# Performance work log

Hardware: AMD Instinct MI355X
Metric: run time of the kernel (lower is better)

The kernel has to match this reference:

```python
import jax, jax.numpy as jnp
import numpy as np

D_INNER, D_STATE, DT_RANK, D_CONV, NBLK = 256, 8, 8, 4, 3

def _conv2d(x, w, b=None):
    y = jax.lax.conv_general_dilated(x, w, (1, 1), 'SAME', dimension_numbers=('NCHW', 'OIHW', 'NCHW'))
    return y if b is None else y + b[None, :, None, None]

def _ln(x, g, b, eps=1e-5):
    m = x.mean(-1, keepdims=True)
    v = x.var(-1, keepdims=True)
    return (x - m) / jnp.sqrt(v + eps) * g + b

def _bn(x, g, b, m, v, eps=1e-5):
    return (x - m[None, :, None, None]) / jnp.sqrt(v[None, :, None, None] + eps) * g[None, :, None, None] + b[None, :, None, None]

def _up2(x):
    return jnp.repeat(jnp.repeat(x, 2, axis=2), 2, axis=3)

def _silu(x):
    return x * jax.nn.sigmoid(x)

def _selective_scan(u, dt, A, Bm, Cm):
    # u, dt: (B,L,D); A: (D,N); Bm, Cm: (B,L,N)
    dA = jnp.exp(dt[..., None] * A)              # (B,L,D,N)
    dBu = (dt * u)[..., None] * Bm[:, :, None, :]
    h0 = jnp.zeros((u.shape[0], u.shape[2], A.shape[1]), u.dtype)
    def step(h, inp):
        dA_t, dBu_t, C_t = inp
        h = dA_t * h + dBu_t
        return h, jnp.einsum('bdn,bn->bd', h, C_t)
    _, ys = jax.lax.scan(step, h0, (jnp.moveaxis(dA, 1, 0), jnp.moveaxis(dBu, 1, 0), jnp.moveaxis(Cm, 1, 0)))
    return jnp.moveaxis(ys, 0, 1)                # (B,L,D)

def _mamba(x, in_w, conv_w, conv_b, xproj_w, dt_w, dt_b, Alog, Dp, out_w):
    xz = jnp.einsum('bld,ed->ble', x, in_w)      # (B,L,2*D_INNER)
    xm, z = jnp.split(xz, 2, axis=-1)
    xc = jnp.moveaxis(xm, 1, 2)                  # (B,D,L)
    xc = jax.lax.conv_general_dilated(xc, conv_w[:, None, :], (1,), [(D_CONV - 1, 0)], dimension_numbers=('NCH', 'OIH', 'NCH'), feature_group_count=D_INNER)
    xm = _silu(jnp.moveaxis(xc + conv_b[None, :, None], 2, 1))
    xdbl = jnp.einsum('bld,ed->ble', xm, xproj_w)
    dt, Bm, Cm = jnp.split(xdbl, [DT_RANK, DT_RANK + D_STATE], axis=-1)
    dt = jax.nn.softplus(jnp.einsum('blr,dr->bld', dt, dt_w) + dt_b)
    A = -jnp.exp(Alog)
    y = _selective_scan(xm, dt, A, Bm, Cm) + xm * Dp
    y = y * _silu(z)
    return jnp.einsum('bld,od->blo', y, out_w)

def _cce(inp, ref, w1, w2):
    a = _conv2d(inp, w1)
    r = _conv2d(ref, w2)
    gate = jax.nn.sigmoid(a.max(axis=(2, 3), keepdims=True) + a.mean(axis=(2, 3), keepdims=True))
    return r * gate


def setup_inputs() -> dict:
    key = jax.random.key(0)
    ks = jax.random.split(key, 24)
    s = 0.05
    inp = {}
    inp['fused'] = jax.random.normal(ks[0], (16, 1024, 128), jnp.float32)
    inp['orig_x'] = jax.random.uniform(ks[1], (16, 32, 128, 128), jnp.float32)
    inp['orig_y'] = jax.random.uniform(ks[2], (16, 32, 128, 128), jnp.float32)
    inp['m_ln_g'] = jnp.ones((NBLK, 128), jnp.float32)
    inp['m_ln_b'] = jnp.zeros((NBLK, 128), jnp.float32)
    inp['m_in_w'] = jax.random.normal(ks[3], (NBLK, 2 * D_INNER, 128), jnp.float32) * s
    inp['m_conv_w'] = jax.random.normal(ks[4], (NBLK, D_INNER, D_CONV), jnp.float32) * s
    inp['m_conv_b'] = jnp.zeros((NBLK, D_INNER), jnp.float32)
    inp['m_xproj_w'] = jax.random.normal(ks[5], (NBLK, DT_RANK + 2 * D_STATE, D_INNER), jnp.float32) * s
    inp['m_dt_w'] = jax.random.normal(ks[6], (NBLK, D_INNER, DT_RANK), jnp.float32) * s
    inp['m_dt_b'] = jax.random.normal(ks[7], (NBLK, D_INNER), jnp.float32) * 0.1
    inp['m_Alog'] = jnp.log(jnp.broadcast_to(jnp.arange(1, D_STATE + 1, dtype=jnp.float32), (NBLK, D_INNER, D_STATE)))
    inp['m_D'] = jnp.ones((NBLK, D_INNER), jnp.float32)
    inp['m_out_w'] = jax.random.normal(ks[8], (NBLK, 128, D_INNER), jnp.float32) * s
    inp['lnf_g'] = jnp.ones((128,), jnp.float32)
    inp['lnf_b'] = jnp.zeros((128,), jnp.float32)
    inp['c1_w'] = jax.random.normal(ks[9], (64, 128, 3, 3), jnp.float32) * s
    inp['c1_b'] = jnp.zeros((64,), jnp.float32)
    inp['bn1_g'] = jnp.ones((64,), jnp.float32)
    inp['bn1_b'] = jnp.zeros((64,), jnp.float32)
    inp['bn1_m'] = jnp.zeros((64,), jnp.float32)
    inp['bn1_v'] = jnp.ones((64,), jnp.float32)
    inp['c2_w'] = jax.random.normal(ks[10], (32, 64, 3, 3), jnp.float32) * s
    inp['c2_b'] = jnp.zeros((32,), jnp.float32)
    inp['bn2_g'] = jnp.ones((32,), jnp.float32)
    inp['bn2_b'] = jnp.zeros((32,), jnp.float32)
    inp['bn2_m'] = jnp.zeros((32,), jnp.float32)
    inp['bn2_v'] = jnp.ones((32,), jnp.float32)
    inp['cce_w1'] = jax.random.normal(ks[11], (32, 32, 1, 1), jnp.float32) * s
    inp['cce_w2'] = jax.random.normal(ks[12], (32, 32, 1, 1), jnp.float32) * s
    inp['c3_w'] = jax.random.normal(ks[13], (1, 32, 3, 3), jnp.float32) * s
    inp['c3_b'] = jnp.zeros((1,), jnp.float32)
    return inp


def reference(fused, orig_x, orig_y, m_ln_g, m_ln_b, m_in_w, m_conv_w, m_conv_b, m_xproj_w, m_dt_w, m_dt_b, m_Alog, m_D, m_out_w, lnf_g, lnf_b, c1_w, c1_b, bn1_g, bn1_b, bn1_m, bn1_v, c2_w, c2_b, bn2_g, bn2_b, bn2_m, bn2_v, cce_w1, cce_w2, c3_w, c3_b):
    # 3 pre-LN Mamba blocks with residual connections
    for i in range(NBLK):
        skip = fused
        h = _ln(fused, m_ln_g[i], m_ln_b[i])
        fused = _mamba(h, m_in_w[i], m_conv_w[i], m_conv_b[i], m_xproj_w[i], m_dt_w[i], m_dt_b[i], m_Alog[i], m_D[i], m_out_w[i]) + skip
    fused = _ln(fused, lnf_g, lnf_b)
    B = fused.shape[0]
    fused = jnp.transpose(fused.reshape(B, 32, 32, 128), (0, 3, 1, 2))  # b c h w
    fused = _up2(fused)
    fused = jax.nn.relu(_bn(_conv2d(fused, c1_w, c1_b), bn1_g, bn1_b, bn1_m, bn1_v))
    fused = _up2(fused)
    fused = _bn(jax.nn.relu(_conv2d(fused, c2_w, c2_b)), bn2_g, bn2_b, bn2_m, bn2_v)
    fused = fused + _cce(orig_x, orig_y, cce_w1, cce_w2)
    fused = fused + _cce(orig_y, orig_x, cce_w1, cce_w2)
    return jax.nn.sigmoid(_conv2d(fused, c3_w, c3_b))
```

## Files before the change

kernel.cpp:

```cpp
#include <hip/hip_runtime.h>
#include <hip/hip_bf16.h>

#define BB   16
#define LL   1024
#define DM   128
#define DIN  256
#define NST  8
#define NROWS (BB*LL)
#define NCH  32
#define TCH  32
#define PSZ  1048576

static __device__ __forceinline__ float sigmoidf_(float x){ return 1.f/(1.f+expf(-x)); }
static __device__ __forceinline__ float siluf_(float x){ return x/(1.f+expf(-x)); }
static __device__ __forceinline__ unsigned short f2bf(float f){
    union { float f; unsigned u; } v; v.f = f;
    unsigned r = v.u + 0x7fff + ((v.u >> 16) & 1);
    return (unsigned short)(r >> 16);
}

typedef __attribute__((ext_vector_type(8))) short short8;
typedef __attribute__((ext_vector_type(4))) float floatx4;

__global__ __launch_bounds__(64) void ln_kernel(const float* __restrict__ X,
        const float* __restrict__ g, const float* __restrict__ b,
        float* __restrict__ Y, int transpose)
{
    int row = blockIdx.x;
    int t = threadIdx.x;
    float x0 = X[(long)row*DM + t];
    float x1 = X[(long)row*DM + 64 + t];
    float s = x0 + x1, ss = x0*x0 + x1*x1;
    #pragma unroll
    for (int off = 32; off; off >>= 1) { s += __shfl_down(s, off); ss += __shfl_down(ss, off); }
    s = __shfl(s, 0); ss = __shfl(ss, 0);
    float mean = s * (1.f/128.f);
    float var  = ss * (1.f/128.f) - mean*mean;
    float inv  = rsqrtf(var + 1e-5f);
    float y0 = (x0-mean)*inv*g[t]    + b[t];
    float y1 = (x1-mean)*inv*g[64+t] + b[64+t];
    if (!transpose) {
        Y[(long)row*DM + t] = y0;
        Y[(long)row*DM + 64 + t] = y1;
    } else {
        int bb = row >> 10, l = row & 1023;
        int r = l >> 5, c = l & 31;
        Y[((long)(bb*DM + t)*34 + (r+1))*34 + (c+1)]      = y0;
        Y[((long)(bb*DM + 64 + t)*34 + (r+1))*34 + (c+1)] = y1;
    }
}

__global__ __launch_bounds__(64) void ln_bf16_kernel(const float* __restrict__ X,
        const float* __restrict__ g, const float* __restrict__ b,
        unsigned short* __restrict__ Y)
{
    int row = blockIdx.x;
    int t = threadIdx.x;
    float x0 = X[(long)row*DM + t];
    float x1 = X[(long)row*DM + 64 + t];
    float s = x0 + x1, ss = x0*x0 + x1*x1;
    #pragma unroll
    for (int off = 32; off; off >>= 1) { s += __shfl_down(s, off); ss += __shfl_down(ss, off); }
    s = __shfl(s, 0); ss = __shfl(ss, 0);
    float mean = s * (1.f/128.f);
    float var  = ss * (1.f/128.f) - mean*mean;
    float inv  = rsqrtf(var + 1e-5f);
    Y[(long)row*DM + t]      = f2bf((x0-mean)*inv*g[t]    + b[t]);
    Y[(long)row*DM + 64 + t] = f2bf((x1-mean)*inv*g[64+t] + b[64+t]);
}

__global__ void wcvt(const float* __restrict__ Win, const float* __restrict__ Wout,
                     unsigned short* __restrict__ Wb)
{
    int t = blockIdx.x*256 + threadIdx.x;
    if (t < 196608) Wb[t] = f2bf(Win[t]);
    else if (t < 294912) Wb[t] = f2bf(Wout[t - 196608]);
}

template<int K, int MT>
__global__ __launch_bounds__(256) void gemm_bf16(const unsigned short* __restrict__ A,
        const unsigned short* __restrict__ Wb, const float* __restrict__ S,
        float* __restrict__ C, int N)
{
    constexpr int NMT = MT/64;
    __shared__ unsigned short Als[MT][40];
    __shared__ unsigned short Bls[128][40];
    const int tid = threadIdx.x;
    const int m0 = blockIdx.x * MT;
    const int n0 = blockIdx.y * 128;
    const int lane = tid & 63, wv = tid >> 6;
    const int fr = lane & 15, quad = lane >> 4;
    floatx4 acc[NMT][8];
    #pragma unroll
    for (int mt = 0; mt < NMT; mt++)
        #pragma unroll
        for (int nt = 0; nt < 8; nt++) acc[mt][nt] = (floatx4){0.f,0.f,0.f,0.f};
    for (int kc = 0; kc < K; kc += 32) {
        __syncthreads();
        #pragma unroll
        for (int u = tid; u < MT*4; u += 256) {
            int row = u >> 2, seg = u & 3;
            *(uint4*)&Als[row][seg*8] = *(const uint4*)&A[(long)(m0+row)*K + kc + seg*8];
        }
        #pragma unroll
        for (int u = tid; u < 512; u += 256) {
            int row = u >> 2, seg = u & 3;
            *(uint4*)&Bls[row][seg*8] = *(const uint4*)&Wb[(long)(n0+row)*K + kc + seg*8];
        }
        __syncthreads();
        short8 af[NMT];
        #pragma unroll
        for (int mt = 0; mt < NMT; mt++)
            af[mt] = *(const short8*)&Als[wv*(16*NMT) + mt*16 + fr][quad*8];
        #pragma unroll
        for (int nt = 0; nt < 8; nt++) {
            short8 bfv = *(const short8*)&Bls[nt*16 + fr][quad*8];
            #pragma unroll
            for (int mt = 0; mt < NMT; mt++)
                acc[mt][nt] = __builtin_amdgcn_mfma_f32_16x16x32_bf16(af[mt], bfv, acc[mt][nt], 0, 0, 0);
        }
    }
    const int rq = quad * 4;
    #pragma unroll
    for (int mt = 0; mt < NMT; mt++)
        #pragma unroll
        for (int nt = 0; nt < 8; nt++)
            #pragma unroll
            for (int r = 0; r < 4; r++) {
                long m = m0 + wv*(16*NMT) + mt*16 + rq + r;
                long n = n0 + nt*16 + fr;
                float v = acc[mt][nt][r];
                if (S) v += S[m*N + n];
                C[m*N + n] = v;
            }
}

#define LT 8
__global__ __launch_bounds__(256) void dwconv_xproj(const float* __restrict__ xz,
        const float* __restrict__ cw, const float* __restrict__ cb,
        const float* __restrict__ xproj_w, const float* __restrict__ dt_w,
        const float* __restrict__ dt_b, float* __restrict__ xc,
        float* __restrict__ dt_out, float* __restrict__ BC)
{
    __shared__ float xstage[LT+3][DIN];
    __shared__ float xs2[LT][DIN];
    __shared__ float xdbl2[LT][24];
    const int idx = blockIdx.x;
    const int b = idx >> 7;
    const int l0 = (idx & 127) * LT;
    const int d = threadIdx.x;
    for (int i = d; i < (LT+3)*DIN; i += 256) {
        int row = i >> 8, dd = i & 255;
        int gl = l0 - 3 + row;
        xstage[row][dd] = (gl >= 0) ? xz[((long)b*LL + gl)*512 + dd] : 0.f;
    }
    float w0 = cw[d*4+0], w1 = cw[d*4+1], w2 = cw[d*4+2], w3 = cw[d*4+3];
    float cbd = cb[d];
    __syncthreads();
    #pragma unroll
    for (int lt = 0; lt < LT; lt++) {
        int l = l0 + lt;
        float acc = cbd + w3 * xstage[lt+3][d];
        if (l >= 1) acc += w2 * xstage[lt+2][d];
        if (l >= 2) acc += w1 * xstage[lt+1][d];
        if (l >= 3) acc += w0 * xstage[lt][d];
        float u = siluf_(acc);
        xs2[lt][d] = u;
        xc[((long)b*LL + l)*DIN + d] = u;
    }
    __syncthreads();
    int t = d;
    if (t < 192) {
        int e = t >> 3, j = t & 7;
        float p[LT];
        #pragma unroll
        for (int lt = 0; lt < LT; lt++) p[lt] = 0.f;
        for (int k = j; k < DIN; k += 8) {
            float w = xproj_w[e*DIN + k];
            #pragma unroll
            for (int lt = 0; lt < LT; lt++) p[lt] += xs2[lt][k] * w;
        }
        #pragma unroll
        for (int lt = 0; lt < LT; lt++) {
            p[lt] += __shfl_down(p[lt], 4, 8);
            p[lt] += __shfl_down(p[lt], 2, 8);
            p[lt] += __shfl_down(p[lt], 1, 8);
        }
        if (j == 0) {
            #pragma unroll
            for (int lt = 0; lt < LT; lt++) xdbl2[lt][e] = p[lt];
        }
    }
    __syncthreads();
    float dw[8];
    #pragma unroll
    for (int r = 0; r < 8; r++) dw[r] = dt_w[d*8 + r];
    float dtbd = dt_b[d];
    #pragma unroll
    for (int lt = 0; lt < LT; lt++) {
        float v = dtbd;
        #pragma unroll
        for (int r = 0; r < 8; r++) v += xdbl2[lt][r] * dw[r];
        v = (v > 20.f) ? v : log1pf(expf(v));
        dt_out[((long)b*LL + l0 + lt)*DIN + d] = v;
    }
    if (t < 128) {
        int lt = t >> 4, j = t & 15;
        BC[((long)b*LL + l0 + lt)*16 + j] = xdbl2[lt][8 + j];
    }
}

__global__ __launch_bounds__(256) void scan_part(const float* __restrict__ dt,
        const float* __restrict__ xc, const float* __restrict__ BC,
        const float* __restrict__ Alog, float* __restrict__ PS)
{
    int b = blockIdx.x, c = blockIdx.y;
    int d = threadIdx.x;
    float a[NST], P[NST], S[NST];
    #pragma unroll
    for (int n = 0; n < NST; n++) { a[n] = -expf(Alog[d*NST + n]); P[n] = 1.f; S[n] = 0.f; }
    int t0 = c*TCH;
    const float* dtp = dt + ((long)b*LL + t0)*DIN + d;
    const float* up  = xc + ((long)b*LL + t0)*DIN + d;
    const float* bc  = BC + ((long)b*LL + t0)*16;
    for (int t = 0; t < TCH; t++) {
        float dtv = dtp[(long)t*DIN];
        float u   = up[(long)t*DIN];
        const float4* bc4 = (const float4*)(bc + t*16);
        float4 B0 = bc4[0], B1 = bc4[1];
        float Bv[NST] = {B0.x,B0.y,B0.z,B0.w,B1.x,B1.y,B1.z,B1.w};
        float dtu = dtv * u;
        #pragma unroll
        for (int n = 0; n < NST; n++) {
            float dA = __expf(dtv * a[n]);
            S[n] = dA * S[n] + dtu * Bv[n];
            P[n] *= dA;
        }
    }
    long o = (((long)b*NCH + c)*DIN + d)*8;
    #pragma unroll
    for (int n = 0; n < NST; n++) { PS[o + n] = P[n]; PS[PSZ + o + n] = S[n]; }
}

__global__ __launch_bounds__(256) void scan_mid(const float* __restrict__ PS,
        float* __restrict__ Hinit)
{
    int b = blockIdx.x;
    int n = blockIdx.y;
    int d = threadIdx.x;
    float h = 0.f;
    for (int c = 0; c < NCH; c++) {
        long o = (((long)b*NCH + c)*DIN + d)*8 + n;
        Hinit[o] = h;
        h = PS[o] * h + PS[PSZ + o];
    }
}

__global__ __launch_bounds__(256) void scan_fin(const float* __restrict__ dt,
        const float* __restrict__ xc, const float* __restrict__ BC,
        const float* __restrict__ xz, const float* __restrict__ Alog,
        const float* __restrict__ Dp, const float* __restrict__ Hinit,
        unsigned short* __restrict__ yg)
{
    int b = blockIdx.x, c = blockIdx.y;
    int d = threadIdx.x;
    float a[NST], h[NST];
    long o = (((long)b*NCH + c)*DIN + d)*8;
    #pragma unroll
    for (int n = 0; n < NST; n++) { a[n] = -expf(Alog[d*NST + n]); h[n] = Hinit[o + n]; }
    float Dpd = Dp[d];
    int t0 = c*TCH;
    const float* dtp = dt + ((long)b*LL + t0)*DIN + d;
    const float* up  = xc + ((long)b*LL + t0)*DIN + d;
    const float* bc  = BC + ((long)b*LL + t0)*16;
    const float* zp  = xz + ((long)b*LL + t0)*512 + 256 + d;
    unsigned short* yo = yg + ((long)b*LL + t0)*DIN + d;
    for (int t = 0; t < TCH; t++) {
        float dtv = dtp[(long)t*DIN];
        float u   = up[(long)t*DIN];
        const float4* bc4 = (const float4*)(bc + t*16);
        float4 B0 = bc4[0], B1 = bc4[1], C0 = bc4[2], C1 = bc4[3];
        float Bv[NST] = {B0.x,B0.y,B0.z,B0.w,B1.x,B1.y,B1.z,B1.w};
        float Cv[NST] = {C0.x,C0.y,C0.z,C0.w,C1.x,C1.y,C1.z,C1.w};
        float dtu = dtv * u;
        float y = 0.f;
        #pragma unroll
        for (int n = 0; n < NST; n++) {
            float dA = __expf(dtv * a[n]);
            h[n] = dA * h[n] + dtu * Bv[n];
            y += h[n] * Cv[n];
        }
        y += u * Dpd;
        float z = zp[(long)t*512];
        yo[(long)t*DIN] = f2bf(y * siluf_(z));
    }
}

__global__ void zpad(float* __restrict__ buf, int NP, int P)
{
    int t = blockIdx.x*256 + threadIdx.x;
    int per = 4*P - 4;
    if (t >= NP*per) return;
    int pl = t / per, k = t % per;
    int r, c;
    if (k < P)        { r = 0;     c = k; }
    else if (k < 2*P) { r = P-1;   c = k - P; }
    else { int kk = k - 2*P; r = 1 + (kk >> 1); c = (kk & 1) ? (P-1) : 0; }
    buf[(long)pl*P*P + (long)r*P + c] = 0.f;
}

__global__ void prep_weff(const float* __restrict__ Wr, float* __restrict__ We, int total)
{
    int t = blockIdx.x*256 + threadIdx.x;
    if (t >= total) return;
    float w[3][3];
    #pragma unroll
    for (int a = 0; a < 3; a++)
        #pragma unroll
        for (int c = 0; c < 3; c++) w[a][c] = Wr[(long)t*9 + a*3 + c];
    float cw[2][3][2];
    #pragma unroll
    for (int ky = 0; ky < 3; ky++) {
        cw[0][ky][0] = w[ky][0];           cw[0][ky][1] = w[ky][1] + w[ky][2];
        cw[1][ky][0] = w[ky][0] + w[ky][1]; cw[1][ky][1] = w[ky][2];
    }
    float* o = We + (long)t*16;
    #pragma unroll
    for (int px = 0; px < 2; px++) {
        o[0*8+px*4+0] = cw[px][0][0];               o[0*8+px*4+1] = cw[px][0][1];
        o[0*8+px*4+2] = cw[px][1][0]+cw[px][2][0];  o[0*8+px*4+3] = cw[px][1][1]+cw[px][2][1];
        o[1*8+px*4+0] = cw[px][0][0]+cw[px][1][0];  o[1*8+px*4+1] = cw[px][0][1]+cw[px][1][1];
        o[1*8+px*4+2] = cw[px][2][0];               o[1*8+px*4+3] = cw[px][2][1];
    }
}

template<int CIN, int INW, int OPAD>
__global__ __launch_bounds__(256) void conv_up2_lw(const float* __restrict__ X,
        const float* __restrict__ We, const float* __restrict__ bias,
        const float* __restrict__ bng, const float* __restrict__ bnb,
        const float* __restrict__ bnm, const float* __restrict__ bnv,
        float* __restrict__ Y, int relu_first, int COUT)
{
    constexpr int OUTW = 2*INW;
    constexpr int NXT  = OUTW/64;
    constexpr int PW   = INW + 2;
    constexpr int OW   = OUTW + 2*OPAD;
    constexpr int ICB  = 32;
    __shared__ float wl[ICB][16][20];
    const int ys = blockIdx.x / NXT, xt = blockIdx.x % NXT;
    const int y0 = ys*8, x0 = xt*64;
    const int ocb = blockIdx.y * 16;
    const int b = blockIdx.z;
    const int tid = threadIdx.x;
    const int rel = tid & 63, ocq = tid >> 6;
    const int Xc = x0 + rel;
    const int px = Xc & 1;
    const int lcp = (rel >> 1) + px;
    float acc[8][4] = {};
    const float* sp = X + (long)(b*CIN)*(PW*PW) + (long)(y0>>1)*PW + (x0>>1) + lcp;
    for (int ic0 = 0; ic0 < CIN; ic0 += ICB) {
        __syncthreads();
        for (int u = tid; u < 2048; u += 256) {
            int ocL = u >> 7, rem = u & 127;
            int icL = rem >> 2, k4 = rem & 3;
            *(float4*)&wl[icL][ocL][k4*4] =
                *(const float4*)&We[((long)(ocb+ocL)*CIN + ic0+icL)*16 + k4*4];
        }
        __syncthreads();
        for (int icL = 0; icL < ICB; icL++) {
            const float* q = sp + (long)(ic0+icL)*(PW*PW);
            float s[6][2];
            #pragma unroll
            for (int r = 0; r < 6; r++) { s[r][0] = q[r*PW]; s[r][1] = q[r*PW + 1]; }
            #pragma unroll
            for (int ol = 0; ol < 4; ol++) {
                float4 w0 = *(const float4*)&wl[icL][(ocq<<2)+ol][px*4];
                float4 w1 = *(const float4*)&wl[icL][(ocq<<2)+ol][8 + px*4];
                #pragma unroll
                for (int p = 0; p < 4; p++) {
                    acc[2*p  ][ol] += w0.x*s[p  ][0] + w0.y*s[p  ][1] + w0.z*s[p+1][0] + w0.w*s[p+1][1];
                    acc[2*p+1][ol] += w1.x*s[p+1][0] + w1.y*s[p+1][1] + w1.z*s[p+2][0] + w1.w*s[p+2][1];
                }
            }
        }
    }
    #pragma unroll
    for (int ol = 0; ol < 4; ol++) {
        int oc = ocb + (ocq<<2) + ol;
        float bi = bias[oc];
        float sc = bng[oc] * rsqrtf(bnv[oc] + 1e-5f);
        float sh = bnb[oc] - bnm[oc]*sc;
        #pragma unroll
        for (int yy = 0; yy < 8; yy++) {
            float v = acc[yy][ol] + bi;
            v = relu_first ? (fmaxf(v, 0.f)*sc + sh) : fmaxf(v*sc + sh, 0.f);
            Y[((long)(b*COUT + oc))*(OW*OW) + (long)(y0+yy+OPAD)*OW + (Xc+OPAD)] = v;
        }
    }
}

__global__ __launch_bounds__(256) void cce_gate_partial(const float* __restrict__ ox,
        const float* __restrict__ oy, const float* __restrict__ w1,
        float* __restrict__ pmax, float* __restrict__ psum)
{
    __shared__ float xs[32*512];
    __shared__ float wl[32*32];
    __shared__ float rmx[4][32], rsm[4][32];
    const int sg = blockIdx.x;
    const int dir = blockIdx.y, b = blockIdx.z;
    const float* X = (dir == 0 ? ox : oy) + (long)b*524288;
    const int t = threadIdx.x;
    for (int i = t; i < 1024; i += 256) { int oc = i >> 5, ic = i & 31; wl[ic*32 + oc] = w1[i]; }
    const int ocg = t & 3, pslot = t >> 2;
    const int oc0 = ocg*8;
    float mx[8], sm[8];
    #pragma unroll
    for (int j = 0; j < 8; j++) { mx[j] = -1e30f; sm[j] = 0.f; }
    const int base = sg*1024;
    for (int tile = 0; tile < 2; tile++) {
        __syncthreads();
        const int p0 = base + tile*512;
        for (int i = t*4; i < 32*512; i += 1024) {
            int ic = i >> 9, px = i & 511;
            *(float4*)&xs[ic*512 + px] = *(const float4*)&X[(long)ic*16384 + p0 + px];
        }
        __syncthreads();
        float acc[8][8];
        #pragma unroll
        for (int p = 0; p < 8; p++)
            #pragma unroll
            for (int j = 0; j < 8; j++) acc[p][j] = 0.f;
        #pragma unroll
        for (int ic = 0; ic < 32; ic++) {
            float4 x0 = *(const float4*)&xs[ic*512 + pslot*4];
            float4 x1 = *(const float4*)&xs[ic*512 + 256 + pslot*4];
            float4 wa = *(const float4*)&wl[ic*32 + oc0];
            float4 wb = *(const float4*)&wl[ic*32 + oc0 + 4];
            float xv[8] = {x0.x,x0.y,x0.z,x0.w,x1.x,x1.y,x1.z,x1.w};
            float wv[8] = {wa.x,wa.y,wa.z,wa.w,wb.x,wb.y,wb.z,wb.w};
            #pragma unroll
            for (int p = 0; p < 8; p++)
                #pragma unroll
                for (int j = 0; j < 8; j++)
                    acc[p][j] += xv[p]*wv[j];
        }
        #pragma unroll
        for (int p = 0; p < 8; p++)
            #pragma unroll
            for (int j = 0; j < 8; j++) { mx[j] = fmaxf(mx[j], acc[p][j]); sm[j] += acc[p][j]; }
    }
    #pragma unroll
    for (int j = 0; j < 8; j++) {
        #pragma unroll
        for (int off = 32; off >= 4; off >>= 1) {
            mx[j] = fmaxf(mx[j], __shfl_down(mx[j], off));
            sm[j] += __shfl_down(sm[j], off);
        }
    }
    const int wave = t >> 6, lane = t & 63;
    __syncthreads();
    if (lane < 4) {
        #pragma unroll
        for (int j = 0; j < 8; j++) { rmx[wave][lane*8+j] = mx[j]; rsm[wave][lane*8+j] = sm[j]; }
    }
    __syncthreads();
    if (t < 32) {
        float M = fmaxf(fmaxf(rmx[0][t], rmx[1][t]), fmaxf(rmx[2][t], rmx[3][t]));
        float S = rsm[0][t] + rsm[1][t] + rsm[2][t] + rsm[3][t];
        long idx = ((long)(dir*16 + b)*32 + t)*16 + sg;
        pmax[idx] = M; psum[idx] = S;
    }
}

__global__ void cce_gate_finish(const float* __restrict__ pmax, const float* __restrict__ psum,
                                float* __restrict__ gates)
{
    int i = blockIdx.x*64 + threadIdx.x;
    if (i < 1024) {
        float M = -1e30f, S = 0.f;
        #pragma unroll
        for (int sg = 0; sg < 16; sg++) { M = fmaxf(M, pmax[i*16+sg]); S += psum[i*16+sg]; }
        gates[i] = sigmoidf_(M + S*(1.f/16384.f));
    }
}

__global__ __launch_bounds__(256) void cce_add(const float* __restrict__ ox,
        const float* __restrict__ oy, const float* __restrict__ w2,
        const float* __restrict__ gates, float* __restrict__ v)
{
    __shared__ float w[32][32];
    int t = threadIdx.x;
    int b = blockIdx.y;
    int s = blockIdx.x*256 + t;
    for (int i = t; i < 1024; i += 256) w[i>>5][i&31] = w2[i];
    __syncthreads();
    const float* xb = ox + (long)b*524288;
    const float* yb = oy + (long)b*524288;
    float r1[32] = {}, r2[32] = {};
    for (int ic = 0; ic < 32; ic++) {
        float xv = xb[(long)ic*16384 + s];
        float yv = yb[(long)ic*16384 + s];
        #pragma unroll
        for (int oc = 0; oc < 32; oc++) { r1[oc] += w[oc][ic]*yv; r2[oc] += w[oc][ic]*xv; }
    }
    float* vb = v + (long)b*524288;
    const float* g1 = gates + b*32;
    const float* g2 = gates + 512 + b*32;
    #pragma unroll
    for (int oc = 0; oc < 32; oc++)
        vb[(long)oc*16384 + s] += g1[oc]*r1[oc] + g2[oc]*r2[oc];
}

__global__ __launch_bounds__(256) void conv3_sig(const float* __restrict__ v,
        const float* __restrict__ w3, const float* __restrict__ b3, float* __restrict__ out)
{
    __shared__ float w[288];
    int t = threadIdx.x;
    for (int i = t; i < 288; i += 256) w[i] = w3[i];
    __syncthreads();
    int b = blockIdx.y;
    int y = blockIdx.x*2 + (t >> 7);
    int x = t & 127;
    const float* vb = v + (long)b*524288;
    float acc = b3[0];
    for (int ic = 0; ic < 32; ic++) {
        const float* p = vb + (long)ic*16384;
        #pragma unroll
        for (int ky = 0; ky < 3; ky++) {
            int yy = y + ky - 1;
            if ((unsigned)yy >= 128u) continue;
            #pragma unroll
            for (int kx = 0; kx < 3; kx++) {
                int xx = x + kx - 1;
                if ((unsigned)xx >= 128u) continue;
                acc += w[ic*9 + ky*3 + kx] * p[yy*128 + xx];
            }
        }
    }
    out[(long)b*16384 + y*128 + x] = sigmoidf_(acc);
}

extern "C" void kernel_launch(void* const* d_in, const int* in_sizes, int n_in,
                              void* d_out, int out_size, void* d_ws, size_t ws_size,
                              hipStream_t stream)
{
    const float* fused_in = (const float*)d_in[0];
    const float* orig_x   = (const float*)d_in[1];
    const float* orig_y   = (const float*)d_in[2];
    const float* m_ln_g   = (const float*)d_in[3];
    const float* m_ln_b   = (const float*)d_in[4];
    const float* m_in_w   = (const float*)d_in[5];
    const float* m_conv_w = (const float*)d_in[6];
    const float* m_conv_b = (const float*)d_in[7];
    const float* m_xproj_w= (const float*)d_in[8];
    const float* m_dt_w   = (const float*)d_in[9];
    const float* m_dt_b   = (const float*)d_in[10];
    const float* m_Alog   = (const float*)d_in[11];
    const float* m_D      = (const float*)d_in[12];
    const float* m_out_w  = (const float*)d_in[13];
    const float* lnf_g    = (const float*)d_in[14];
    const float* lnf_b    = (const float*)d_in[15];
    const float* c1_w     = (const float*)d_in[16];
    const float* c1_b     = (const float*)d_in[17];
    const float* bn1_g    = (const float*)d_in[18];
    const float* bn1_b    = (const float*)d_in[19];
    const float* bn1_m    = (const float*)d_in[20];
    const float* bn1_v    = (const float*)d_in[21];
    const float* c2_w     = (const float*)d_in[22];
    const float* c2_b     = (const float*)d_in[23];
    const float* bn2_g    = (const float*)d_in[24];
    const float* bn2_b    = (const float*)d_in[25];
    const float* bn2_m    = (const float*)d_in[26];
    const float* bn2_v    = (const float*)d_in[27];
    const float* cce_w1   = (const float*)d_in[28];
    const float* cce_w2   = (const float*)d_in[29];
    const float* c3_w     = (const float*)d_in[30];
    const float* c3_b     = (const float*)d_in[31];

    float* W = (float*)d_ws;
    float* fusedA = W;
    float* fusedB = W + 2097152;
    float* xzb    = W + 4194304;
    float* xcb    = W + 12582912;
    float* dtb    = W + 16777216;
    float* ygb    = W + 20971520;
    float* BCb    = W + 25165824;
    float* gates  = W + 25427968;
    float* Hinit  = W + 25445376;
    float* pmax   = W + 26493952;
    float* psum   = W + 26510336;
    unsigned short* xlnb = (unsigned short*)ygb;
    unsigned short* ygbb = (unsigned short*)ygb;
    unsigned short* wbf  = ((unsigned short*)ygb) + 4194304;
    float* tb_pad  = xzb;
    float* c1b_pad = xzb + 2367488;
    float* vb  = dtb;
    float* weff1 = BCb;
    float* weff2 = BCb + 131072;

    cce_gate_partial<<<dim3(16,2,16), 256, 0, stream>>>(orig_x, orig_y, cce_w1, pmax, psum);
    cce_gate_finish<<<16, 64, 0, stream>>>(pmax, psum, gates);

    wcvt<<<1152, 256, 0, stream>>>(m_in_w, m_out_w, wbf);

    const float* cur = fused_in;
    float* nxt = fusedA;
    for (int i = 0; i < 3; i++) {
        ln_bf16_kernel<<<NROWS, 64, 0, stream>>>(cur, m_ln_g + i*128, m_ln_b + i*128, xlnb);
        gemm_bf16<128,128><<<dim3(128, 4), 256, 0, stream>>>(xlnb, wbf + (long)i*65536, nullptr, xzb, 512);
        dwconv_xproj<<<2048, 256, 0, stream>>>(xzb, m_conv_w + i*1024, m_conv_b + i*256,
                m_xproj_w + i*24*256, m_dt_w + i*2048, m_dt_b + i*256, xcb, dtb, BCb);
        scan_part<<<dim3(BB, NCH), 256, 0, stream>>>(dtb, xcb, BCb, m_Alog + i*2048, nxt);
        scan_mid<<<dim3(BB, NST), 256, 0, stream>>>(nxt, Hinit);
        scan_fin<<<dim3(BB, NCH), 256, 0, stream>>>(dtb, xcb, BCb, xzb, m_Alog + i*2048, m_D + i*256, Hinit, ygbb);
        gemm_bf16<256,64><<<dim3(256, 1), 256, 0, stream>>>(ygbb, wbf + 196608 + (long)i*32768, cur, nxt, 128);
        cur = nxt;
        nxt = (i == 0) ? fusedB : fusedA;
    }
    zpad<<<1056, 256, 0, stream>>>(tb_pad, 2048, 34);
    zpad<<<1040, 256, 0, stream>>>(c1b_pad, 1024, 66);
    ln_kernel<<<NROWS, 64, 0, stream>>>(cur, lnf_g, lnf_b, tb_pad, 1);
    prep_weff<<<32, 256, 0, stream>>>(c1_w, weff1, 64*128);
    prep_weff<<<8, 256, 0, stream>>>(c2_w, weff2, 32*64);
    conv_up2_lw<128, 32, 1><<<dim3(8, 4, 16), 256, 0, stream>>>(tb_pad, weff1, c1_b, bn1_g, bn1_b, bn1_m, bn1_v, c1b_pad, 0, 64);
    conv_up2_lw<64, 64, 0><<<dim3(32, 2, 16), 256, 0, stream>>>(c1b_pad, weff2, c2_b, bn2_g, bn2_b, bn2_m, bn2_v, vb, 1, 32);
    cce_add<<<dim3(64, 16), 256, 0, stream>>>(orig_x, orig_y, cce_w2, gates, vb);
    conv3_sig<<<dim3(64, 16), 256, 0, stream>>>(vb, c3_w, c3_b, (float*)d_out);
}
```

Before: 788.3 us.

## Fuse LayerNorm into in-proj GEMM and selective-scan finish into out-proj GEMM

The per-block LayerNorm is folded into the in-projection GEMM: each block computes row mean and inverse std for its 128 rows, then normalises and converts to bf16 while staging the A tile in shared memory. The scan finish step now writes its gated bf16 outputs for a 32-step chunk into shared memory and immediately multiplies them by the out-projection weights, adding the residual. This removes two kernel launches per layer and the global round trips of the normalised activations and the scan output. In exchange, LN statistics are recomputed by each of the four N-tile blocks, and every scan block reloads the full out-projection weight from L2.

New measurement: 802.1 us. Within noise of the previous version (+1.8%).

```diff
diff --git a/kernel.cpp b/kernel.cpp
--- a/kernel.cpp
+++ b/kernel.cpp
@@ -50,25 +50,6 @@
     }
 }
 
-__global__ __launch_bounds__(64) void ln_bf16_kernel(const float* __restrict__ X,
-        const float* __restrict__ g, const float* __restrict__ b,
-        unsigned short* __restrict__ Y)
-{
-    int row = blockIdx.x;
-    int t = threadIdx.x;
-    float x0 = X[(long)row*DM + t];
-    float x1 = X[(long)row*DM + 64 + t];
-    float s = x0 + x1, ss = x0*x0 + x1*x1;
-    #pragma unroll
-    for (int off = 32; off; off >>= 1) { s += __shfl_down(s, off); ss += __shfl_down(ss, off); }
-    s = __shfl(s, 0); ss = __shfl(ss, 0);
-    float mean = s * (1.f/128.f);
-    float var  = ss * (1.f/128.f) - mean*mean;
-    float inv  = rsqrtf(var + 1e-5f);
-    Y[(long)row*DM + t]      = f2bf((x0-mean)*inv*g[t]    + b[t]);
-    Y[(long)row*DM + 64 + t] = f2bf((x1-mean)*inv*g[64+t] + b[64+t]);
-}
-
 __global__ void wcvt(const float* __restrict__ Win, const float* __restrict__ Wout,
                      unsigned short* __restrict__ Wb)
 {
@@ -77,61 +58,83 @@
     else if (t < 294912) Wb[t] = f2bf(Wout[t - 196608]);
 }
 
-template<int K, int MT>
-__global__ __launch_bounds__(256) void gemm_bf16(const unsigned short* __restrict__ A,
-        const unsigned short* __restrict__ Wb, const float* __restrict__ S,
-        float* __restrict__ C, int N)
-{
-    constexpr int NMT = MT/64;
-    __shared__ unsigned short Als[MT][40];
+__global__ __launch_bounds__(256) void gemm_ln_bf16(const float* __restrict__ X,
+        const float* __restrict__ g, const float* __restrict__ b,
+        const unsigned short* __restrict__ Wb, float* __restrict__ C, int N)
+{
+    __shared__ unsigned short Als[128][40];
     __shared__ unsigned short Bls[128][40];
+    __shared__ float rowm[128], rowi[128], gls[128], bls2[128];
     const int tid = threadIdx.x;
-    const int m0 = blockIdx.x * MT;
+    const int m0 = blockIdx.x * 128;
     const int n0 = blockIdx.y * 128;
     const int lane = tid & 63, wv = tid >> 6;
     const int fr = lane & 15, quad = lane >> 4;
-    floatx4 acc[NMT][8];
-    #pragma unroll
-    for (int mt = 0; mt < NMT; mt++)
+    if (tid < 128) { gls[tid] = g[tid]; bls2[tid] = b[tid]; }
+    for (int i = 0; i < 32; i++) {
+        int row = wv*32 + i;
+        float x0 = X[(long)(m0+row)*DM + lane];
+        float x1 = X[(long)(m0+row)*DM + 64 + lane];
+        float s = x0 + x1, ss = x0*x0 + x1*x1;
+        #pragma unroll
+        for (int off = 32; off; off >>= 1) { s += __shfl_down(s, off); ss += __shfl_down(ss, off); }
+        s = __shfl(s, 0); ss = __shfl(ss, 0);
+        float mean = s * (1.f/128.f);
+        float var  = ss * (1.f/128.f) - mean*mean;
+        float inv  = rsqrtf(var + 1e-5f);
+        if (lane == 0) { rowm[row] = mean; rowi[row] = inv; }
+    }
+    floatx4 acc[2][8];
+    #pragma unroll
+    for (int mt = 0; mt < 2; mt++)
         #pragma unroll
         for (int nt = 0; nt < 8; nt++) acc[mt][nt] = (floatx4){0.f,0.f,0.f,0.f};
-    for (int kc = 0; kc < K; kc += 32) {
-        __syncthreads();
-        #pragma unroll
-        for (int u = tid; u < MT*4; u += 256) {
-            int row = u >> 2, seg = u & 3;
-            *(uint4*)&Als[row][seg*8] = *(const uint4*)&A[(long)(m0+row)*K + kc + seg*8];
-        }
+    for (int kc = 0; kc < 128; kc += 32) {
+        __syncthreads();
         #pragma unroll
         for (int u = tid; u < 512; u += 256) {
             int row = u >> 2, seg = u & 3;
-            *(uint4*)&Bls[row][seg*8] = *(const uint4*)&Wb[(long)(n0+row)*K + kc + seg*8];
-        }
-        __syncthreads();
-        short8 af[NMT];
-        #pragma unroll
-        for (int mt = 0; mt < NMT; mt++)
-            af[mt] = *(const short8*)&Als[wv*(16*NMT) + mt*16 + fr][quad*8];
+            float m_ = rowm[row], iv = rowi[row];
+            const float* xp = &X[(long)(m0+row)*DM + kc + seg*8];
+            float4 a0 = *(const float4*)xp;
+            float4 a1 = *(const float4*)(xp + 4);
+            const float* gp = &gls[kc + seg*8];
+            const float* bp = &bls2[kc + seg*8];
+            unsigned h0 = (unsigned)f2bf((a0.x-m_)*iv*gp[0]+bp[0]) | ((unsigned)f2bf((a0.y-m_)*iv*gp[1]+bp[1]) << 16);
+            unsigned h1 = (unsigned)f2bf((a0.z-m_)*iv*gp[2]+bp[2]) | ((unsigned)f2bf((a0.w-m_)*iv*gp[3]+bp[3]) << 16);
+            unsigned h2 = (unsigned)f2bf((a1.x-m_)*iv*gp[4]+bp[4]) | ((unsigned)f2bf((a1.y-m_)*iv*gp[5]+bp[5]) << 16);
+            unsigned h3 = (unsigned)f2bf((a1.z-m_)*iv*gp[6]+bp[6]) | ((unsigned)f2bf((a1.w-m_)*iv*gp[7]+bp[7]) << 16);
+            uint4 pk; pk.x = h0; pk.y = h1; pk.z = h2; pk.w = h3;
+            *(uint4*)&Als[row][seg*8] = pk;
+        }
+        #pragma unroll
+        for (int u = tid; u < 512; u += 256) {
+            int row = u >> 2, seg = u & 3;
+            *(uint4*)&Bls[row][seg*8] = *(const uint4*)&Wb[(long)(n0+row)*128 + kc + seg*8];
+        }
+        __syncthreads();
+        short8 af[2];
+        #pragma unroll
+        for (int mt = 0; mt < 2; mt++)
+            af[mt] = *(const short8*)&Als[wv*32 + mt*16 + fr][quad*8];
         #pragma unroll
         for (int nt = 0; nt < 8; nt++) {
             short8 bfv = *(const short8*)&Bls[nt*16 + fr][quad*8];
             #pragma unroll
-            for (int mt = 0; mt < NMT; mt++)
+            for (int mt = 0; mt < 2; mt++)
                 acc[mt][nt] = __builtin_amdgcn_mfma_f32_16x16x32_bf16(af[mt], bfv, acc[mt][nt], 0, 0, 0);
         }
     }
     const int rq = quad * 4;
     #pragma unroll
-    for (int mt = 0; mt < NMT; mt++)
+    for (int mt = 0; mt < 2; mt++)
         #pragma unroll
         for (int nt = 0; nt < 8; nt++)
             #pragma unroll
             for (int r = 0; r < 4; r++) {
-                long m = m0 + wv*(16*NMT) + mt*16 + rq + r;
+                long m = m0 + wv*32 + mt*16 + rq + r;
                 long n = n0 + nt*16 + fr;
-                float v = acc[mt][nt][r];
-                if (S) v += S[m*N + n];
-                C[m*N + n] = v;
+                C[m*N + n] = acc[mt][nt][r];
             }
 }
 
@@ -256,44 +259,89 @@
     }
 }
 
-__global__ __launch_bounds__(256) void scan_fin(const float* __restrict__ dt,
+__global__ __launch_bounds__(256) void scanfin_gemm(const float* __restrict__ dt,
         const float* __restrict__ xc, const float* __restrict__ BC,
         const float* __restrict__ xz, const float* __restrict__ Alog,
         const float* __restrict__ Dp, const float* __restrict__ Hinit,
-        unsigned short* __restrict__ yg)
-{
+        const unsigned short* __restrict__ Wb, const float* __restrict__ S,
+        float* __restrict__ C)
+{
+    __shared__ unsigned short ygl[32][264];
+    __shared__ unsigned short Wls[128][40];
     int b = blockIdx.x, c = blockIdx.y;
     int d = threadIdx.x;
-    float a[NST], h[NST];
-    long o = (((long)b*NCH + c)*DIN + d)*8;
-    #pragma unroll
-    for (int n = 0; n < NST; n++) { a[n] = -expf(Alog[d*NST + n]); h[n] = Hinit[o + n]; }
-    float Dpd = Dp[d];
-    int t0 = c*TCH;
-    const float* dtp = dt + ((long)b*LL + t0)*DIN + d;
-    const float* up  = xc + ((long)b*LL + t0)*DIN + d;
-    const float* bc  = BC + ((long)b*LL + t0)*16;
-    const float* zp  = xz + ((long)b*LL + t0)*512 + 256 + d;
-    unsigned short* yo = yg + ((long)b*LL + t0)*DIN + d;
-    for (int t = 0; t < TCH; t++) {
-        float dtv = dtp[(long)t*DIN];
-        float u   = up[(long)t*DIN];
-        const float4* bc4 = (const float4*)(bc + t*16);
-        float4 B0 = bc4[0], B1 = bc4[1], C0 = bc4[2], C1 = bc4[3];
-        float Bv[NST] = {B0.x,B0.y,B0.z,B0.w,B1.x,B1.y,B1.z,B1.w};
-        float Cv[NST] = {C0.x,C0.y,C0.z,C0.w,C1.x,C1.y,C1.z,C1.w};
-        float dtu = dtv * u;
-        float y = 0.f;
-        #pragma unroll
-        for (int n = 0; n < NST; n++) {
-            float dA = __expf(dtv * a[n]);
-            h[n] = dA * h[n] + dtu * Bv[n];
-            y += h[n] * Cv[n];
-        }
-        y += u * Dpd;
-        float z = zp[(long)t*512];
-        yo[(long)t*DIN] = f2bf(y * siluf_(z));
-    }
+    {
+        float a[NST], h[NST];
+        long o = (((long)b*NCH + c)*DIN + d)*8;
+        #pragma unroll
+        for (int n = 0; n < NST; n++) { a[n] = -expf(Alog[d*NST + n]); h[n] = Hinit[o + n]; }
+        float Dpd = Dp[d];
+        int t0 = c*TCH;
+        const float* dtp = dt + ((long)b*LL + t0)*DIN + d;
+        const float* up  = xc + ((long)b*LL + t0)*DIN + d;
+        const float* bc  = BC + ((long)b*LL + t0)*16;
+        const float* zp  = xz + ((long)b*LL + t0)*512 + 256 + d;
+        for (int t = 0; t < TCH; t++) {
+            float dtv = dtp[(long)t*DIN];
+            float u   = up[(long)t*DIN];
+            const float4* bc4 = (const float4*)(bc + t*16);
+            float4 B0 = bc4[0], B1 = bc4[1], C0 = bc4[2], C1 = bc4[3];
+            float Bv[NST] = {B0.x,B0.y,B0.z,B0.w,B1.x,B1.y,B1.z,B1.w};
+            float Cv[NST] = {C0.x,C0.y,C0.z,C0.w,C1.x,C1.y,C1.z,C1.w};
+            float dtu = dtv * u;
+            float y = 0.f;
+            #pragma unroll
+            for (int n = 0; n < NST; n++) {
+                float dA = __expf(dtv * a[n]);
+                h[n] = dA * h[n] + dtu * Bv[n];
+                y += h[n] * Cv[n];
+            }
+            y += u * Dpd;
+            float z = zp[(long)t*512];
+            ygl[t][d] = f2bf(y * siluf_(z));
+        }
+    }
+    __syncthreads();
+    const int tid = d;
+    const int lane = tid & 63, wv = tid >> 6;
+    const int fr = lane & 15, quad = lane >> 4;
+    floatx4 acc[2][2];
+    #pragma unroll
+    for (int mt = 0; mt < 2; mt++)
+        #pragma unroll
+        for (int nt = 0; nt < 2; nt++) acc[mt][nt] = (floatx4){0.f,0.f,0.f,0.f};
+    for (int kc = 0; kc < 256; kc += 32) {
+        __syncthreads();
+        #pragma unroll
+        for (int u = tid; u < 512; u += 256) {
+            int row = u >> 2, seg = u & 3;
+            *(uint4*)&Wls[row][seg*8] = *(const uint4*)&Wb[(long)row*256 + kc + seg*8];
+        }
+        __syncthreads();
+        short8 af[2];
+        #pragma unroll
+        for (int mt = 0; mt < 2; mt++)
+            af[mt] = *(const short8*)&ygl[mt*16 + fr][kc + quad*8];
+        #pragma unroll
+        for (int ntl = 0; ntl < 2; ntl++) {
+            short8 bfv = *(const short8*)&Wls[(wv*2+ntl)*16 + fr][quad*8];
+            #pragma unroll
+            for (int mt = 0; mt < 2; mt++)
+                acc[mt][ntl] = __builtin_amdgcn_mfma_f32_16x16x32_bf16(af[mt], bfv, acc[mt][ntl], 0, 0, 0);
+        }
+    }
+    const int rq = quad * 4;
+    const int t0 = c*TCH;
+    #pragma unroll
+    for (int mt = 0; mt < 2; mt++)
+        #pragma unroll
+        for (int ntl = 0; ntl < 2; ntl++)
+            #pragma unroll
+            for (int r = 0; r < 4; r++) {
+                long m = (long)b*LL + t0 + mt*16 + rq + r;
+                long n = (wv*2+ntl)*16 + fr;
+                C[m*128 + n] = acc[mt][ntl][r] + S[m*128 + n];
+            }
 }
 
 __global__ void zpad(float* __restrict__ buf, int NP, int P)
@@ -589,8 +637,6 @@
     float* Hinit  = W + 25445376;
     float* pmax   = W + 26493952;
     float* psum   = W + 26510336;
-    unsigned short* xlnb = (unsigned short*)ygb;
-    unsigned short* ygbb = (unsigned short*)ygb;
     unsigned short* wbf  = ((unsigned short*)ygb) + 4194304;
     float* tb_pad  = xzb;
     float* c1b_pad = xzb + 2367488;
@@ -606,14 +652,14 @@
     const float* cur = fused_in;
     float* nxt = fusedA;
     for (int i = 0; i < 3; i++) {
-        ln_bf16_kernel<<<NROWS, 64, 0, stream>>>(cur, m_ln_g + i*128, m_ln_b + i*128, xlnb);
-        gemm_bf16<128,128><<<dim3(128, 4), 256, 0, stream>>>(xlnb, wbf + (long)i*65536, nullptr, xzb, 512);
+        gemm_ln_bf16<<<dim3(128, 4), 256, 0, stream>>>(cur, m_ln_g + i*128, m_ln_b + i*128,
+                wbf + (long)i*65536, xzb, 512);
         dwconv_xproj<<<2048, 256, 0, stream>>>(xzb, m_conv_w + i*1024, m_conv_b + i*256,
                 m_xproj_w + i*24*256, m_dt_w + i*2048, m_dt_b + i*256, xcb, dtb, BCb);
         scan_part<<<dim3(BB, NCH), 256, 0, stream>>>(dtb, xcb, BCb, m_Alog + i*2048, nxt);
         scan_mid<<<dim3(BB, NST), 256, 0, stream>>>(nxt, Hinit);
-        scan_fin<<<dim3(BB, NCH), 256, 0, stream>>>(dtb, xcb, BCb, xzb, m_Alog + i*2048, m_D + i*256, Hinit, ygbb);
-        gemm_bf16<256,64><<<dim3(256, 1), 256, 0, stream>>>(ygbb, wbf + 196608 + (long)i*32768, cur, nxt, 128);
+        scanfin_gemm<<<dim3(BB, NCH), 256, 0, stream>>>(dtb, xcb, BCb, xzb, m_Alog + i*2048,
+                m_D + i*256, Hinit, wbf + 196608 + (long)i*32768, cur, nxt);
         cur = nxt;
         nxt = (i == 0) ? fusedB : fusedA;
     }
```
